# Kernel optimization log

Hardware: AMD Instinct MI355X
Metric: run time of the kernel (lower is better)

## Reference

```python
import jax, jax.numpy as jnp
import numpy as np

B, H, W, C = 8, 224, 224, 96
WS = 7            # window size
NH = 3            # num heads
HD = C // NH      # head dim = 32
N = WS * WS       # tokens per window = 49
SCALE = HD ** -0.5


def _relative_position_index():
    coords = np.stack(np.meshgrid(np.arange(WS), np.arange(WS), indexing='ij'))  # (2,WS,WS)
    flat = coords.reshape(2, -1)                      # (2, N)
    rel = flat[:, :, None] - flat[:, None, :]          # (2, N, N)
    rel = rel.transpose(1, 2, 0).astype(np.int32)      # (N, N, 2)
    rel[:, :, 0] += WS - 1
    rel[:, :, 1] += WS - 1
    rel[:, :, 0] *= 2 * WS - 1
    return rel.sum(-1)                                 # (N, N) in [0, (2WS-1)^2)


def window_partition(x):
    # x: (B,H,W,C) -> (B*nW, WS*WS, C)
    b, h, w, c = x.shape
    x = x.reshape(b, h // WS, WS, w // WS, WS, c)
    x = x.transpose(0, 1, 3, 2, 4, 5)
    return x.reshape(-1, WS * WS, c)


def window_reverse(win, h, w):
    b = win.shape[0] // ((h // WS) * (w // WS))
    x = win.reshape(b, h // WS, w // WS, WS, WS, -1)
    x = x.transpose(0, 1, 3, 2, 4, 5)
    return x.reshape(b, h, w, -1)


def layernorm(x, g, b, eps=1e-5):
    mu = jnp.mean(x, axis=-1, keepdims=True)
    var = jnp.var(x, axis=-1, keepdims=True)
    return (x - mu) * jax.lax.rsqrt(var + eps) * g + b


def setup_inputs() -> dict:
    key = jax.random.key(0)
    ks = jax.random.split(key, 8)
    std = 0.02
    rpe_table_size = (2 * WS - 1) * (2 * WS - 1)  # 169
    return {
        'rescaled': jax.random.normal(ks[0], (B, H * W, C), jnp.float32),
        'rescaler': jax.random.normal(ks[1], (B, H * W, C), jnp.float32),
        'norm_w_a': jnp.ones((C,), jnp.float32),
        'norm_b_a': jnp.zeros((C,), jnp.float32),
        'norm_w_b': jnp.ones((C,), jnp.float32),
        'norm_b_b': jnp.zeros((C,), jnp.float32),
        'qkv_w_a': jax.random.normal(ks[2], (C, 3 * C), jnp.float32) * std,
        'qkv_b_a': jnp.zeros((3 * C,), jnp.float32),
        'qkv_w_b': jax.random.normal(ks[3], (C, 3 * C), jnp.float32) * std,
        'qkv_b_b': jnp.zeros((3 * C,), jnp.float32),
        'rpe_table': jax.random.normal(ks[4], (NH, rpe_table_size), jnp.float32) * std,
        'proj_w': jax.random.normal(ks[5], (C, C), jnp.float32) * std,
        'proj_b': jnp.zeros((C,), jnp.float32),
        'rpe_index': jnp.asarray(_relative_position_index(), jnp.int32),
    }


def reference(rescaled, rescaler, norm_w_a, norm_b_a, norm_w_b, norm_b_b,
              qkv_w_a, qkv_b_a, qkv_w_b, qkv_b_b, rpe_table, proj_w, proj_b,
              rpe_index):
    # BeforeCrossAttention for each stream (shift_size=0): LN -> window partition
    def before(x, g, b):
        x = layernorm(x, g, b)
        x = x.reshape(B, H, W, C)
        return window_partition(x)                   # (B*nW, N, C)

    xa = before(rescaled, norm_w_a, norm_b_a)        # rescaled stream
    xb = before(rescaler, norm_w_b, norm_b_b)        # rescaler stream
    Bw = xa.shape[0]                                 # B * nW windows

    def qkv(x, wq, bq):
        o = x @ wq + bq                              # (Bw, N, 3C)
        o = o.reshape(Bw, N, 3, NH, HD)
        return jnp.moveaxis(o, 2, 0)                 # (3, Bw, NH, N, HD) after transpose

    qkv_a = qkv(xa, qkv_w_a, qkv_b_a).transpose(0, 1, 3, 2, 4)  # (3,Bw,NH,N,HD)
    qkv_b = qkv(xb, qkv_w_b, qkv_b_b).transpose(0, 1, 3, 2, 4)

    # same_key_query=False: q from rescaler, k/v from rescaled
    q = qkv_b[0] * SCALE
    k = qkv_a[1]
    v = qkv_a[2]

    rpe = rpe_table[:, rpe_index]                    # (NH, N, N) relative position bias
    attn = jnp.einsum('whnd,whmd->whnm', q, k) + rpe # (Bw, NH, N, N)
    attn = jax.nn.softmax(attn, axis=-1)
    out = jnp.einsum('whnm,whmd->whnd', attn, v)     # (Bw, NH, N, HD)
    out = out.transpose(0, 2, 1, 3).reshape(Bw, N, C)
    out = out @ proj_w + proj_b
    out = window_reverse(out, H, W)                  # (B, H, W, C)
    return out.reshape(B, H * W, C)
```

## Files before the change

### kernel.cpp

```cpp
#include <hip/hip_runtime.h>
#include <hip/hip_bf16.h>

#define DI __device__ __forceinline__

typedef __bf16 bf16x8 __attribute__((ext_vector_type(8)));
typedef float f32x4 __attribute__((ext_vector_type(4)));

constexpr float SCALE_Q = 0.17677669529663687f;

constexpr int WQKV_OFF = 0;
constexpr int WVLO_OFF = 55296;
constexpr int WPRJ_OFF = 73728;
constexpr int BIAS_OFF = 92160;
constexpr int RPE_OFF  = 93696;

DI unsigned int f2b(float x) {
  union { float f; unsigned int u; } v; v.f = x;
  return (v.u + 0x7fffu + ((v.u >> 16) & 1u)) >> 16;
}
DI unsigned int f2bh(float x) {
  union { __bf16 b; unsigned short u; } v;
  v.b = (__bf16)x;
  return (unsigned int)v.u;
}
DI float b2f(unsigned int u) {
  union { unsigned int u; float f; } v; v.u = u << 16;
  return v.f;
}
DI int sw192(int row, int bytecol) { return (row * 192 + bytecol) ^ ((row & 7) << 4); }

__global__ void prepack_kernel(const float* __restrict__ qkv_w_a,
                               const float* __restrict__ qkv_b_a,
                               const float* __restrict__ qkv_w_b,
                               const float* __restrict__ qkv_b_b,
                               const float* __restrict__ rpe_table,
                               const float* __restrict__ proj_w,
                               const float* __restrict__ proj_b,
                               const int* __restrict__ rpe_index,
                               unsigned char* __restrict__ ws)
{
  unsigned short* wqkv = (unsigned short*)(ws + WQKV_OFF);
  unsigned short* wvlo = (unsigned short*)(ws + WVLO_OFF);
  unsigned short* wprj = (unsigned short*)(ws + WPRJ_OFF);
  float* bias          = (float*)(ws + BIAS_OFF);
  unsigned short* rpe  = (unsigned short*)(ws + RPE_OFF);

  const int total = 27648 + 9216 + 9216 + 384 + 12288;
  for (int idx = blockIdx.x * blockDim.x + threadIdx.x; idx < total;
       idx += gridDim.x * blockDim.x) {
    int i = idx;
    if (i < 27648) {
      const int j = i & 7, lane = (i >> 3) & 63, t = i >> 9;
      const int kt = t % 3, nt = t / 3;
      const int k = kt * 32 + (lane >> 4) * 8 + j, c = lane & 15;
      float v;
      if (nt < 12) v = qkv_w_a[k * 288 + 96 + nt * 16 + c];
      else         v = qkv_w_b[k * 288 + (nt - 12) * 16 + c] * SCALE_Q;
      wqkv[i] = (unsigned short)f2b(v);
    } else if ((i -= 27648) < 9216) {
      const int j = i & 7, lane = (i >> 3) & 63, t = i >> 9;
      const int kt = t % 3, vnt = t / 3;
      const int k = kt * 32 + (lane >> 4) * 8 + j, c = lane & 15;
      const float full = qkv_w_a[k * 288 + 192 + vnt * 16 + c];
      const unsigned int hi = f2b(full);
      wvlo[i] = (unsigned short)f2b(full - b2f(hi));
    } else if ((i -= 9216) < 9216) {
      const int j = i & 7, lane = (i >> 3) & 63, t = i >> 9;
      const int kt = t % 3, nt = t / 3;
      const int k = kt * 32 + (lane >> 4) * 8 + j, c = lane & 15;
      wprj[i] = (unsigned short)f2b(proj_w[k * 96 + nt * 16 + c]);
    } else if ((i -= 9216) < 384) {
      float v;
      if (i < 192)      v = qkv_b_a[96 + i];
      else if (i < 288) v = qkv_b_b[i - 192] * SCALE_Q;
      else              v = proj_b[i - 288];
      bias[i] = v;
    } else {
      i -= 384;
      const int h = i >> 12, rest = i & 4095;
      const int qrow = rest >> 6, lg = (rest >> 4) & 3, mt = (rest >> 2) & 3, r = i & 3;
      const int key = mt * 16 + lg * 4 + r;
      float v;
      if (key >= 49)       v = -1e30f;
      else if (qrow >= 49) v = 0.f;
      else                 v = rpe_table[h * 169 + rpe_index[qrow * 49 + key]];
      rpe[i] = (unsigned short)f2b(v);
    }
  }
}

__global__ __launch_bounds__(256, 3)
void swin_main(const float* __restrict__ xa_in, const float* __restrict__ xb_in,
               const float* __restrict__ nwa, const float* __restrict__ nba,
               const float* __restrict__ nwb, const float* __restrict__ nbb,
               const unsigned char* __restrict__ ws, float* __restrict__ out)
{
  __shared__ unsigned char smem[53248];
  unsigned char* const R0 = smem;
  unsigned char* const R1 = smem + 12288;
  unsigned char* const R2 = smem + 24576;
  unsigned char* const PB = smem + 36864;
  unsigned char* const OB = smem + 45056;

  const int tid = threadIdx.x;
  const int w   = tid >> 6;
  const int l   = tid & 63;
  const int l15 = l & 15;
  const int lg  = l >> 4;

  const int bw  = blockIdx.x;
  const int bb  = bw >> 10;
  const int hwi = (bw >> 5) & 31;
  const int wwi = bw & 31;
  const int pixbase = (bb * 224 + hwi * 7) * 224 + wwi * 7;

  const f32x4 zf = {0.f, 0.f, 0.f, 0.f};

  {
    const int tok = tid >> 2;
    const int j   = tid & 3;
    const int ch0 = j * 24;
    if (tok < 49) {
      const int gbase = (pixbase + (tok / 7) * 224 + (tok % 7)) * 96 + ch0;
      auto doLN = [&](const float* __restrict__ xin, const float* __restrict__ gw,
                      const float* __restrict__ gb, unsigned char* dstHi,
                      unsigned char* dstLo) {
        float x[24];
        float s = 0.f, s2 = 0.f;
#pragma unroll
        for (int t = 0; t < 6; ++t) {
          const float4 v = *(const float4*)(xin + gbase + t * 4);
          x[t*4+0] = v.x; x[t*4+1] = v.y; x[t*4+2] = v.z; x[t*4+3] = v.w;
          s  += v.x + v.y + v.z + v.w;
          s2 += v.x*v.x + v.y*v.y + v.z*v.z + v.w*v.w;
        }
        s += __shfl_xor(s, 1);  s2 += __shfl_xor(s2, 1);
        s += __shfl_xor(s, 2);  s2 += __shfl_xor(s2, 2);
        const float mu = s * (1.f / 96.f);
        const float rs = rsqrtf(s2 * (1.f / 96.f) - mu * mu + 1e-5f);
        unsigned int hi[12], lo[12];
#pragma unroll
        for (int t = 0; t < 6; ++t) {
          const float4 g  = *(const float4*)(gw + ch0 + t * 4);
          const float4 be = *(const float4*)(gb + ch0 + t * 4);
          const float y0 = (x[t*4+0] - mu) * rs * g.x + be.x;
          const float y1 = (x[t*4+1] - mu) * rs * g.y + be.y;
          const float y2 = (x[t*4+2] - mu) * rs * g.z + be.z;
          const float y3 = (x[t*4+3] - mu) * rs * g.w + be.w;
          const unsigned int h0 = f2bh(y0), h1 = f2bh(y1), h2 = f2bh(y2), h3 = f2bh(y3);
          hi[t*2+0] = h0 | (h1 << 16);
          hi[t*2+1] = h2 | (h3 << 16);
          if (dstLo) {
            const unsigned int l0 = f2bh(y0 - b2f(h0)), l1 = f2bh(y1 - b2f(h1));
            const unsigned int l2 = f2bh(y2 - b2f(h2)), l3 = f2bh(y3 - b2f(h3));
            lo[t*2+0] = l0 | (l1 << 16);
            lo[t*2+1] = l2 | (l3 << 16);
          }
        }
#pragma unroll
        for (int p = 0; p < 3; ++p) {
          const int off = sw192(tok, (ch0 + p * 8) * 2);
          uint4 uh = {hi[p*4+0], hi[p*4+1], hi[p*4+2], hi[p*4+3]};
          *(uint4*)(dstHi + off) = uh;
          if (dstLo) {
            uint4 ul = {lo[p*4+0], lo[p*4+1], lo[p*4+2], lo[p*4+3]};
            *(uint4*)(dstLo + off) = ul;
          }
        }
      };
      doLN(xa_in, nwa, nba, R0, R2);
      doLN(xb_in, nwb, nbb, R1, nullptr);
    } else {
      const uint4 z = {0u, 0u, 0u, 0u};
#pragma unroll
      for (int p = 0; p < 3; ++p) {
        const int off = sw192(tok, (ch0 + p * 8) * 2);
        *(uint4*)(R0 + off) = z; *(uint4*)(R1 + off) = z; *(uint4*)(R2 + off) = z;
      }
    }
  }
  __syncthreads();

  {
    const float* bias = (const float*)(ws + BIAS_OFF);
    f32x4 acc[5][4];
#pragma unroll
    for (int i = 0; i < 5; ++i) {
      const int nt = w + 4 * i;
      const float bv = (nt < 18) ? bias[nt * 16 + l15] : 0.f;
      const f32x4 bvv = {bv, bv, bv, bv};
#pragma unroll
      for (int m = 0; m < 4; ++m) acc[i][m] = bvv;
    }

    const unsigned char* wqkv = ws + WQKV_OFF;
    const unsigned char* wvlo = ws + WVLO_OFF;

    for (int kt = 0; kt < 3; ++kt) {
      bf16x8 axa[4], axb[4], axlo[4];
      const int abyte = kt * 64 + lg * 16;
#pragma unroll
      for (int mt = 0; mt < 4; ++mt) {
        const int row = mt * 16 + l15;
        const int off = sw192(row, abyte);
        axa[mt]  = *(const bf16x8*)(R0 + off);
        axb[mt]  = *(const bf16x8*)(R1 + off);
        axlo[mt] = *(const bf16x8*)(R2 + off);
      }
#pragma unroll
      for (int i = 0; i < 5; ++i) {
        const int nt = w + 4 * i;
        if (nt < 18) {
          const bf16x8 bw_ = *(const bf16x8*)(wqkv + ((nt * 3 + kt) * 64 + l) * 16);
          if (nt >= 6 && nt < 12) {
            const bf16x8 bl = *(const bf16x8*)(wvlo + (((nt - 6) * 3 + kt) * 64 + l) * 16);
#pragma unroll
            for (int mt = 0; mt < 4; ++mt) {
              acc[i][mt] = __builtin_amdgcn_mfma_f32_16x16x32_bf16(axa[mt],  bw_, acc[i][mt], 0, 0, 0);
              acc[i][mt] = __builtin_amdgcn_mfma_f32_16x16x32_bf16(axlo[mt], bw_, acc[i][mt], 0, 0, 0);
              acc[i][mt] = __builtin_amdgcn_mfma_f32_16x16x32_bf16(axa[mt],  bl,  acc[i][mt], 0, 0, 0);
            }
          } else if (nt >= 12) {
#pragma unroll
            for (int mt = 0; mt < 4; ++mt)
              acc[i][mt] = __builtin_amdgcn_mfma_f32_16x16x32_bf16(axb[mt], bw_, acc[i][mt], 0, 0, 0);
          } else {
#pragma unroll
            for (int mt = 0; mt < 4; ++mt)
              acc[i][mt] = __builtin_amdgcn_mfma_f32_16x16x32_bf16(axa[mt], bw_, acc[i][mt], 0, 0, 0);
          }
        }
      }
    }
    __syncthreads();

#pragma unroll
    for (int i = 0; i < 5; ++i) {
      const int nt = w + 4 * i;
      if (nt < 6) {
        const int col = nt * 16 + l15;
#pragma unroll
        for (int mt = 0; mt < 4; ++mt)
#pragma unroll
          for (int r = 0; r < 4; ++r) {
            const int row = mt * 16 + lg * 4 + r;
            *(unsigned short*)(R0 + sw192(row, col * 2)) = (unsigned short)f2bh(acc[i][mt][r]);
          }
      }
    }
#pragma unroll
    for (int i = 0; i < 5; ++i) {
      const int nt = w + 4 * i;
      if (nt >= 12 && nt < 18) {
        const int col = (nt - 12) * 16 + l15;
#pragma unroll
        for (int mt = 0; mt < 4; ++mt)
#pragma unroll
          for (int r = 0; r < 4; ++r) {
            const int row = mt * 16 + lg * 4 + r;
            *(unsigned short*)(R1 + sw192(row, col * 2)) = (unsigned short)f2bh(acc[i][mt][r]);
          }
      }
    }
#pragma unroll
    for (int i = 0; i < 5; ++i) {
      const int nt = w + 4 * i;
      if (nt >= 6 && nt < 12) {
        const int dim = (nt - 6) * 16 + l15;
#pragma unroll
        for (int mt = 0; mt < 4; ++mt) {
          const int key0 = mt * 16 + lg * 4;
          const unsigned int u0 = f2bh(acc[i][mt][0]) | (f2bh(acc[i][mt][1]) << 16);
          const unsigned int u1 = f2bh(acc[i][mt][2]) | (f2bh(acc[i][mt][3]) << 16);
          uint2 u = {u0, u1};
          *(uint2*)(R2 + ((dim * 128 + key0 * 2) ^ ((dim & 7) << 4))) = u;
        }
      }
    }
  }
  __syncthreads();

  f32x4 po[6];
  {
    const float* bias = (const float*)(ws + BIAS_OFF);
#pragma unroll
    for (int nt = 0; nt < 6; ++nt) {
      const float bv = bias[288 + nt * 16 + l15];
      po[nt] = {bv, bv, bv, bv};
    }

    const unsigned short* rpe = (const unsigned short*)(ws + RPE_OFF);
    const int qrow = w * 16 + l15;
    const int qsz  = (qrow & 7) << 4;

    uint2 rp[3][4];
#pragma unroll
    for (int h = 0; h < 3; ++h)
#pragma unroll
      for (int mt = 0; mt < 4; ++mt)
        rp[h][mt] = *(const uint2*)(rpe + (h * 4096 + qrow * 64 + lg * 16 + mt * 4));

    const unsigned char* wp = ws + WPRJ_OFF;

#pragma unroll
    for (int h = 0; h < 3; ++h) {
      const bf16x8 qB = *(const bf16x8*)(R1 + sw192(qrow, h * 64 + lg * 16));
      f32x4 sT[4];
#pragma unroll
      for (int mt = 0; mt < 4; ++mt) {
        const bf16x8 kA = *(const bf16x8*)(R0 + sw192(mt * 16 + l15, h * 64 + lg * 16));
        sT[mt] = __builtin_amdgcn_mfma_f32_16x16x32_bf16(kA, qB, zf, 0, 0, 0);
      }
      float e[16];
#pragma unroll
      for (int mt = 0; mt < 4; ++mt) {
        const uint2 u = rp[h][mt];
        e[mt*4+0] = sT[mt][0] + b2f(u.x & 0xffffu);
        e[mt*4+1] = sT[mt][1] + b2f(u.x >> 16);
        e[mt*4+2] = sT[mt][2] + b2f(u.y & 0xffffu);
        e[mt*4+3] = sT[mt][3] + b2f(u.y >> 16);
      }
      float mx = e[0];
#pragma unroll
      for (int i = 1; i < 16; ++i) mx = fmaxf(mx, e[i]);
      mx = fmaxf(mx, __shfl_xor(mx, 16));
      mx = fmaxf(mx, __shfl_xor(mx, 32));
      float sm = 0.f;
#pragma unroll
      for (int i = 0; i < 16; ++i) { e[i] = __expf(e[i] - mx); sm += e[i]; }
      sm += __shfl_xor(sm, 16);
      sm += __shfl_xor(sm, 32);
      const float inv = __fdividef(1.f, sm);

#pragma unroll
      for (int mt = 0; mt < 4; ++mt) {
        uint2 u;
        u.x = f2bh(e[mt*4+0]) | (f2bh(e[mt*4+1]) << 16);
        u.y = f2bh(e[mt*4+2]) | (f2bh(e[mt*4+3]) << 16);
        *(uint2*)(PB + ((qrow * 128 + mt * 32 + lg * 8) ^ qsz)) = u;
      }

      f32x4 od0 = zf, od1 = zf;
      const int d0 = h * 32 + l15;
      const int d1 = d0 + 16;
#pragma unroll
      for (int blk = 0; blk < 2; ++blk) {
        const bf16x8 pf = *(const bf16x8*)(PB + ((qrow * 128 + blk * 64 + lg * 16) ^ qsz));
        const bf16x8 v0 = *(const bf16x8*)(R2 + ((d0 * 128 + blk * 64 + lg * 16) ^ ((d0 & 7) << 4)));
        const bf16x8 v1 = *(const bf16x8*)(R2 + ((d1 * 128 + blk * 64 + lg * 16) ^ ((d1 & 7) << 4)));
        od0 = __builtin_amdgcn_mfma_f32_16x16x32_bf16(v0, pf, od0, 0, 0, 0);
        od1 = __builtin_amdgcn_mfma_f32_16x16x32_bf16(v1, pf, od1, 0, 0, 0);
      }

      {
        uint2 o0p, o1p;
        o0p.x = f2bh(od0[0] * inv) | (f2bh(od0[1] * inv) << 16);
        o0p.y = f2bh(od0[2] * inv) | (f2bh(od0[3] * inv) << 16);
        o1p.x = f2bh(od1[0] * inv) | (f2bh(od1[1] * inv) << 16);
        o1p.y = f2bh(od1[2] * inv) | (f2bh(od1[3] * inv) << 16);
        *(uint2*)(OB + ((qrow * 128 +      lg * 8) ^ qsz)) = o0p;
        *(uint2*)(OB + ((qrow * 128 + 32 + lg * 8) ^ qsz)) = o1p;
      }
      const bf16x8 af = *(const bf16x8*)(OB + ((qrow * 128 + lg * 16) ^ qsz));

#pragma unroll
      for (int nt = 0; nt < 6; ++nt) {
        const bf16x8 bp = *(const bf16x8*)(wp + ((nt * 3 + h) * 64 + l) * 16);
        po[nt] = __builtin_amdgcn_mfma_f32_16x16x32_bf16(af, bp, po[nt], 0, 0, 0);
      }
    }
  }

  {
#pragma unroll
    for (int r = 0; r < 4; ++r) {
      const int row = w * 16 + lg * 4 + r;
      if (row < 49) {
        const int pix = pixbase + (row / 7) * 224 + (row % 7);
        float* dst = out + (long)pix * 96 + l15;
#pragma unroll
        for (int nt = 0; nt < 6; ++nt)
          dst[nt * 16] = po[nt][r];
      }
    }
  }
}

extern "C" void kernel_launch(void* const* d_in, const int* in_sizes, int n_in,
                              void* d_out, int out_size, void* d_ws, size_t ws_size,
                              hipStream_t stream)
{
  const float* rescaled  = (const float*)d_in[0];
  const float* rescaler  = (const float*)d_in[1];
  const float* norm_w_a  = (const float*)d_in[2];
  const float* norm_b_a  = (const float*)d_in[3];
  const float* norm_w_b  = (const float*)d_in[4];
  const float* norm_b_b  = (const float*)d_in[5];
  const float* qkv_w_a   = (const float*)d_in[6];
  const float* qkv_b_a   = (const float*)d_in[7];
  const float* qkv_w_b   = (const float*)d_in[8];
  const float* qkv_b_b   = (const float*)d_in[9];
  const float* rpe_table = (const float*)d_in[10];
  const float* proj_w    = (const float*)d_in[11];
  const float* proj_b    = (const float*)d_in[12];
  const int*   rpe_index = (const int*)d_in[13];
  unsigned char* ws = (unsigned char*)d_ws;
  float* outp = (float*)d_out;

  hipLaunchKernelGGL(prepack_kernel, dim3(64), dim3(256), 0, stream,
                     qkv_w_a, qkv_b_a, qkv_w_b, qkv_b_b, rpe_table, proj_w,
                     proj_b, rpe_index, ws);
  hipLaunchKernelGGL(swin_main, dim3(8192), dim3(256), 0, stream,
                     rescaled, rescaler, norm_w_a, norm_b_a, norm_w_b, norm_b_b,
                     ws, outp);
}
```

Measured before the change: 228.8 us.

## Compact LDS layout and split QKV GEMM to fit four blocks per CU

Shared memory shrinks from 53 KB to about 39 KB and the launch bound rises from 3 to 4 blocks per CU. To get there, activation buffers are packed to 49 rows so that their padding rows overlap the next buffer, the attention-output buffer reuses the probability buffer, and only the tail of the last buffer is explicitly zeroed. The QKV projection is split into a K/V phase and a separate Q phase, cutting live accumulators from 20 to 12 tiles to reduce register pressure, at the cost of an extra barrier. Both input streams are now loaded together before LayerNorm for more memory-level parallelism. The padded rows now read neighbouring data instead of zeros, which relies on the bias mask and the discarded output rows to stay correct.

```diff
diff --git a/kernel.cpp b/kernel.cpp
--- a/kernel.cpp
+++ b/kernel.cpp
@@ -13,6 +13,11 @@
 constexpr int WPRJ_OFF = 73728;
 constexpr int BIAS_OFF = 92160;
 constexpr int RPE_OFF  = 93696;
+
+constexpr int XA_OFF  = 0;
+constexpr int XB_OFF  = 9408;
+constexpr int XLO_OFF = 18816;
+constexpr int PB_OFF  = 31104;
 
 DI unsigned int f2b(float x) {
   union { float f; unsigned int u; } v; v.f = x;
@@ -89,18 +94,13 @@
   }
 }
 
-__global__ __launch_bounds__(256, 3)
+__global__ __launch_bounds__(256, 4)
 void swin_main(const float* __restrict__ xa_in, const float* __restrict__ xb_in,
                const float* __restrict__ nwa, const float* __restrict__ nba,
                const float* __restrict__ nwb, const float* __restrict__ nbb,
                const unsigned char* __restrict__ ws, float* __restrict__ out)
 {
-  __shared__ unsigned char smem[53248];
-  unsigned char* const R0 = smem;
-  unsigned char* const R1 = smem + 12288;
-  unsigned char* const R2 = smem + 24576;
-  unsigned char* const PB = smem + 36864;
-  unsigned char* const OB = smem + 45056;
+  __shared__ unsigned char smem[39296];
 
   const int tid = threadIdx.x;
   const int w   = tid >> 6;
@@ -122,17 +122,23 @@
     const int ch0 = j * 24;
     if (tok < 49) {
       const int gbase = (pixbase + (tok / 7) * 224 + (tok % 7)) * 96 + ch0;
-      auto doLN = [&](const float* __restrict__ xin, const float* __restrict__ gw,
+      float xa_[24], xb_[24];
+#pragma unroll
+      for (int t = 0; t < 6; ++t) {
+        const float4 va = *(const float4*)(xa_in + gbase + t * 4);
+        const float4 vb = *(const float4*)(xb_in + gbase + t * 4);
+        xa_[t*4+0] = va.x; xa_[t*4+1] = va.y; xa_[t*4+2] = va.z; xa_[t*4+3] = va.w;
+        xb_[t*4+0] = vb.x; xb_[t*4+1] = vb.y; xb_[t*4+2] = vb.z; xb_[t*4+3] = vb.w;
+      }
+      auto doLN = [&](const float* x, const float* __restrict__ gw,
                       const float* __restrict__ gb, unsigned char* dstHi,
                       unsigned char* dstLo) {
-        float x[24];
         float s = 0.f, s2 = 0.f;
 #pragma unroll
         for (int t = 0; t < 6; ++t) {
-          const float4 v = *(const float4*)(xin + gbase + t * 4);
-          x[t*4+0] = v.x; x[t*4+1] = v.y; x[t*4+2] = v.z; x[t*4+3] = v.w;
-          s  += v.x + v.y + v.z + v.w;
-          s2 += v.x*v.x + v.y*v.y + v.z*v.z + v.w*v.w;
+          s  += x[t*4+0] + x[t*4+1] + x[t*4+2] + x[t*4+3];
+          s2 += x[t*4+0]*x[t*4+0] + x[t*4+1]*x[t*4+1]
+              + x[t*4+2]*x[t*4+2] + x[t*4+3]*x[t*4+3];
         }
         s += __shfl_xor(s, 1);  s2 += __shfl_xor(s2, 1);
         s += __shfl_xor(s, 2);  s2 += __shfl_xor(s2, 2);
@@ -168,74 +174,65 @@
           }
         }
       };
-      doLN(xa_in, nwa, nba, R0, R2);
-      doLN(xb_in, nwb, nbb, R1, nullptr);
+      doLN(xa_, nwa, nba, smem + XA_OFF, smem + XLO_OFF);
+      doLN(xb_, nwb, nbb, smem + XB_OFF, nullptr);
     } else {
+      const int o = 28224 + (tid - 196) * 48;
       const uint4 z = {0u, 0u, 0u, 0u};
-#pragma unroll
-      for (int p = 0; p < 3; ++p) {
-        const int off = sw192(tok, (ch0 + p * 8) * 2);
-        *(uint4*)(R0 + off) = z; *(uint4*)(R1 + off) = z; *(uint4*)(R2 + off) = z;
-      }
+      *(uint4*)(smem + o)      = z;
+      *(uint4*)(smem + o + 16) = z;
+      *(uint4*)(smem + o + 32) = z;
     }
   }
   __syncthreads();
 
   {
     const float* bias = (const float*)(ws + BIAS_OFF);
-    f32x4 acc[5][4];
-#pragma unroll
-    for (int i = 0; i < 5; ++i) {
-      const int nt = w + 4 * i;
-      const float bv = (nt < 18) ? bias[nt * 16 + l15] : 0.f;
-      const f32x4 bvv = {bv, bv, bv, bv};
-#pragma unroll
-      for (int m = 0; m < 4; ++m) acc[i][m] = bvv;
-    }
-
     const unsigned char* wqkv = ws + WQKV_OFF;
     const unsigned char* wvlo = ws + WVLO_OFF;
 
+    f32x4 acc[3][4];
+#pragma unroll
+    for (int i = 0; i < 3; ++i) {
+      const int nt = w + 4 * i;
+      const float bv = bias[nt * 16 + l15];
+      const f32x4 bvv = {bv, bv, bv, bv};
+#pragma unroll
+      for (int m = 0; m < 4; ++m) acc[i][m] = bvv;
+    }
+
     for (int kt = 0; kt < 3; ++kt) {
-      bf16x8 axa[4], axb[4], axlo[4];
+      bf16x8 axa[4], axlo[4];
       const int abyte = kt * 64 + lg * 16;
 #pragma unroll
       for (int mt = 0; mt < 4; ++mt) {
-        const int row = mt * 16 + l15;
-        const int off = sw192(row, abyte);
-        axa[mt]  = *(const bf16x8*)(R0 + off);
-        axb[mt]  = *(const bf16x8*)(R1 + off);
-        axlo[mt] = *(const bf16x8*)(R2 + off);
-      }
-#pragma unroll
-      for (int i = 0; i < 5; ++i) {
+        const int off = sw192(mt * 16 + l15, abyte);
+        axa[mt]  = *(const bf16x8*)(smem + XA_OFF + off);
+        axlo[mt] = *(const bf16x8*)(smem + XLO_OFF + off);
+      }
+#pragma unroll
+      for (int i = 0; i < 3; ++i) {
         const int nt = w + 4 * i;
-        if (nt < 18) {
-          const bf16x8 bw_ = *(const bf16x8*)(wqkv + ((nt * 3 + kt) * 64 + l) * 16);
-          if (nt >= 6 && nt < 12) {
-            const bf16x8 bl = *(const bf16x8*)(wvlo + (((nt - 6) * 3 + kt) * 64 + l) * 16);
-#pragma unroll
-            for (int mt = 0; mt < 4; ++mt) {
-              acc[i][mt] = __builtin_amdgcn_mfma_f32_16x16x32_bf16(axa[mt],  bw_, acc[i][mt], 0, 0, 0);
-              acc[i][mt] = __builtin_amdgcn_mfma_f32_16x16x32_bf16(axlo[mt], bw_, acc[i][mt], 0, 0, 0);
-              acc[i][mt] = __builtin_amdgcn_mfma_f32_16x16x32_bf16(axa[mt],  bl,  acc[i][mt], 0, 0, 0);
-            }
-          } else if (nt >= 12) {
-#pragma unroll
-            for (int mt = 0; mt < 4; ++mt)
-              acc[i][mt] = __builtin_amdgcn_mfma_f32_16x16x32_bf16(axb[mt], bw_, acc[i][mt], 0, 0, 0);
-          } else {
-#pragma unroll
-            for (int mt = 0; mt < 4; ++mt)
-              acc[i][mt] = __builtin_amdgcn_mfma_f32_16x16x32_bf16(axa[mt], bw_, acc[i][mt], 0, 0, 0);
+        const bf16x8 bw_ = *(const bf16x8*)(wqkv + ((nt * 3 + kt) * 64 + l) * 16);
+        if (nt >= 6) {
+          const bf16x8 bl = *(const bf16x8*)(wvlo + (((nt - 6) * 3 + kt) * 64 + l) * 16);
+#pragma unroll
+          for (int mt = 0; mt < 4; ++mt) {
+            acc[i][mt] = __builtin_amdgcn_mfma_f32_16x16x32_bf16(axa[mt],  bw_, acc[i][mt], 0, 0, 0);
+            acc[i][mt] = __builtin_amdgcn_mfma_f32_16x16x32_bf16(axlo[mt], bw_, acc[i][mt], 0, 0, 0);
+            acc[i][mt] = __builtin_amdgcn_mfma_f32_16x16x32_bf16(axa[mt],  bl,  acc[i][mt], 0, 0, 0);
           }
+        } else {
+#pragma unroll
+          for (int mt = 0; mt < 4; ++mt)
+            acc[i][mt] = __builtin_amdgcn_mfma_f32_16x16x32_bf16(axa[mt], bw_, acc[i][mt], 0, 0, 0);
         }
       }
     }
     __syncthreads();
 
 #pragma unroll
-    for (int i = 0; i < 5; ++i) {
+    for (int i = 0; i < 2; ++i) {
       const int nt = w + 4 * i;
       if (nt < 6) {
         const int col = nt * 16 + l15;
@@ -244,28 +241,16 @@
 #pragma unroll
           for (int r = 0; r < 4; ++r) {
             const int row = mt * 16 + lg * 4 + r;
-            *(unsigned short*)(R0 + sw192(row, col * 2)) = (unsigned short)f2bh(acc[i][mt][r]);
+            if (row < 49)
+              *(unsigned short*)(smem + XA_OFF + sw192(row, col * 2)) =
+                  (unsigned short)f2bh(acc[i][mt][r]);
           }
       }
     }
 #pragma unroll
-    for (int i = 0; i < 5; ++i) {
+    for (int i = 1; i < 3; ++i) {
       const int nt = w + 4 * i;
-      if (nt >= 12 && nt < 18) {
-        const int col = (nt - 12) * 16 + l15;
-#pragma unroll
-        for (int mt = 0; mt < 4; ++mt)
-#pragma unroll
-          for (int r = 0; r < 4; ++r) {
-            const int row = mt * 16 + lg * 4 + r;
-            *(unsigned short*)(R1 + sw192(row, col * 2)) = (unsigned short)f2bh(acc[i][mt][r]);
-          }
-      }
-    }
-#pragma unroll
-    for (int i = 0; i < 5; ++i) {
-      const int nt = w + 4 * i;
-      if (nt >= 6 && nt < 12) {
+      if (nt >= 6) {
         const int dim = (nt - 6) * 16 + l15;
 #pragma unroll
         for (int mt = 0; mt < 4; ++mt) {
@@ -273,8 +258,59 @@
           const unsigned int u0 = f2bh(acc[i][mt][0]) | (f2bh(acc[i][mt][1]) << 16);
           const unsigned int u1 = f2bh(acc[i][mt][2]) | (f2bh(acc[i][mt][3]) << 16);
           uint2 u = {u0, u1};
-          *(uint2*)(R2 + ((dim * 128 + key0 * 2) ^ ((dim & 7) << 4))) = u;
-        }
+          *(uint2*)(smem + XLO_OFF + ((dim * 128 + key0 * 2) ^ ((dim & 7) << 4))) = u;
+        }
+      }
+    }
+  }
+
+  {
+    const float* bias = (const float*)(ws + BIAS_OFF);
+    const unsigned char* wqkv = ws + WQKV_OFF;
+
+    f32x4 acq[2][4];
+#pragma unroll
+    for (int i = 0; i < 2; ++i) {
+      const int nt = w + 12 + 4 * i;
+      const float bv = (nt < 18) ? bias[nt * 16 + l15] : 0.f;
+      const f32x4 bvv = {bv, bv, bv, bv};
+#pragma unroll
+      for (int m = 0; m < 4; ++m) acq[i][m] = bvv;
+    }
+
+    for (int kt = 0; kt < 3; ++kt) {
+      bf16x8 axb[4];
+      const int abyte = kt * 64 + lg * 16;
+#pragma unroll
+      for (int mt = 0; mt < 4; ++mt)
+        axb[mt] = *(const bf16x8*)(smem + XB_OFF + sw192(mt * 16 + l15, abyte));
+#pragma unroll
+      for (int i = 0; i < 2; ++i) {
+        const int nt = w + 12 + 4 * i;
+        if (nt < 18) {
+          const bf16x8 bw_ = *(const bf16x8*)(wqkv + ((nt * 3 + kt) * 64 + l) * 16);
+#pragma unroll
+          for (int mt = 0; mt < 4; ++mt)
+            acq[i][mt] = __builtin_amdgcn_mfma_f32_16x16x32_bf16(axb[mt], bw_, acq[i][mt], 0, 0, 0);
+        }
+      }
+    }
+    __syncthreads();
+
+#pragma unroll
+    for (int i = 0; i < 2; ++i) {
+      const int nt = w + 12 + 4 * i;
+      if (nt < 18) {
+        const int col = (nt - 12) * 16 + l15;
+#pragma unroll
+        for (int mt = 0; mt < 4; ++mt)
+#pragma unroll
+          for (int r = 0; r < 4; ++r) {
+            const int row = mt * 16 + lg * 4 + r;
+            if (row < 49)
+              *(unsigned short*)(smem + XB_OFF + sw192(row, col * 2)) =
+                  (unsigned short)f2bh(acq[i][mt][r]);
+          }
       }
     }
   }
@@ -304,11 +340,11 @@
 
 #pragma unroll
     for (int h = 0; h < 3; ++h) {
-      const bf16x8 qB = *(const bf16x8*)(R1 + sw192(qrow, h * 64 + lg * 16));
+      const bf16x8 qB = *(const bf16x8*)(smem + XB_OFF + sw192(qrow, h * 64 + lg * 16));
       f32x4 sT[4];
 #pragma unroll
       for (int mt = 0; mt < 4; ++mt) {
-        const bf16x8 kA = *(const bf16x8*)(R0 + sw192(mt * 16 + l15, h * 64 + lg * 16));
+        const bf16x8 kA = *(const bf16x8*)(smem + XA_OFF + sw192(mt * 16 + l15, h * 64 + lg * 16));
         sT[mt] = __builtin_amdgcn_mfma_f32_16x16x32_bf16(kA, qB, zf, 0, 0, 0);
       }
       float e[16];
@@ -337,7 +373,7 @@
         uint2 u;
         u.x = f2bh(e[mt*4+0]) | (f2bh(e[mt*4+1]) << 16);
         u.y = f2bh(e[mt*4+2]) | (f2bh(e[mt*4+3]) << 16);
-        *(uint2*)(PB + ((qrow * 128 + mt * 32 + lg * 8) ^ qsz)) = u;
+        *(uint2*)(smem + PB_OFF + ((qrow * 128 + mt * 32 + lg * 8) ^ qsz)) = u;
       }
 
       f32x4 od0 = zf, od1 = zf;
@@ -345,9 +381,9 @@
       const int d1 = d0 + 16;
 #pragma unroll
       for (int blk = 0; blk < 2; ++blk) {
-        const bf16x8 pf = *(const bf16x8*)(PB + ((qrow * 128 + blk * 64 + lg * 16) ^ qsz));
-        const bf16x8 v0 = *(const bf16x8*)(R2 + ((d0 * 128 + blk * 64 + lg * 16) ^ ((d0 & 7) << 4)));
-        const bf16x8 v1 = *(const bf16x8*)(R2 + ((d1 * 128 + blk * 64 + lg * 16) ^ ((d1 & 7) << 4)));
+        const bf16x8 pf = *(const bf16x8*)(smem + PB_OFF + ((qrow * 128 + blk * 64 + lg * 16) ^ qsz));
+        const bf16x8 v0 = *(const bf16x8*)(smem + XLO_OFF + ((d0 * 128 + blk * 64 + lg * 16) ^ ((d0 & 7) << 4)));
+        const bf16x8 v1 = *(const bf16x8*)(smem + XLO_OFF + ((d1 * 128 + blk * 64 + lg * 16) ^ ((d1 & 7) << 4)));
         od0 = __builtin_amdgcn_mfma_f32_16x16x32_bf16(v0, pf, od0, 0, 0, 0);
         od1 = __builtin_amdgcn_mfma_f32_16x16x32_bf16(v1, pf, od1, 0, 0, 0);
       }
@@ -358,10 +394,10 @@
         o0p.y = f2bh(od0[2] * inv) | (f2bh(od0[3] * inv) << 16);
         o1p.x = f2bh(od1[0] * inv) | (f2bh(od1[1] * inv) << 16);
         o1p.y = f2bh(od1[2] * inv) | (f2bh(od1[3] * inv) << 16);
-        *(uint2*)(OB + ((qrow * 128 +      lg * 8) ^ qsz)) = o0p;
-        *(uint2*)(OB + ((qrow * 128 + 32 + lg * 8) ^ qsz)) = o1p;
-      }
-      const bf16x8 af = *(const bf16x8*)(OB + ((qrow * 128 + lg * 16) ^ qsz));
+        *(uint2*)(smem + PB_OFF + ((qrow * 128 +      lg * 8) ^ qsz)) = o0p;
+        *(uint2*)(smem + PB_OFF + ((qrow * 128 + 32 + lg * 8) ^ qsz)) = o1p;
+      }
+      const bf16x8 af = *(const bf16x8*)(smem + PB_OFF + ((qrow * 128 + lg * 16) ^ qsz));
 
 #pragma unroll
       for (int nt = 0; nt < 6; ++nt) {
```

Measured after the change: 188.6 us. -17.6%, faster.
